# Kernel tuning notes

Hardware: AMD Instinct MI355X
Metric: run time of the kernel (lower is better)

## Reference

```python
import jax, jax.numpy as jnp
import numpy as np

HID = 1024
HEADS = 16
HEAD_DIM = HID // HEADS
MLP_HID = 4096
TEMB = 1024
EPS = 1e-6


def _ln(x):
    # LayerNorm without affine, eps=1e-6
    mu = jnp.mean(x, axis=-1, keepdims=True)
    var = jnp.var(x, axis=-1, keepdims=True)
    return (x - mu) * jax.lax.rsqrt(var + EPS)


def _modulate(x, shift, scale):
    return x * (1.0 + scale[:, None, :]) + shift[:, None, :]


def setup_inputs() -> dict:
    key = jax.random.key(0)
    ks = jax.random.split(key, 12)
    s = 0.02
    return {
        "x": jax.random.normal(ks[0], (8, 1024, HID), jnp.float32),
        "c": jax.random.normal(ks[1], (8, TEMB), jnp.float32),
        "W_qkv": jax.random.normal(ks[2], (HID, 3 * HID), jnp.float32) * s,
        "b_qkv": jnp.zeros((3 * HID,), jnp.float32),
        "W_proj": jax.random.normal(ks[3], (HID, HID), jnp.float32) * s,
        "b_proj": jnp.zeros((HID,), jnp.float32),
        "W_fc1": jax.random.normal(ks[4], (HID, MLP_HID), jnp.float32) * s,
        "b_fc1": jnp.zeros((MLP_HID,), jnp.float32),
        "W_fc2": jax.random.normal(ks[5], (MLP_HID, HID), jnp.float32) * s,
        "b_fc2": jnp.zeros((HID,), jnp.float32),
        "W_ada": jax.random.normal(ks[6], (TEMB, 6 * HID), jnp.float32) * s,
        "b_ada": jnp.zeros((6 * HID,), jnp.float32),
    }


def _attn(x, W_qkv, b_qkv, W_proj, b_proj):
    B, N, C = x.shape
    qkv = x @ W_qkv + b_qkv                      # [B,N,3C]
    qkv = qkv.reshape(B, N, 3, HEADS, HEAD_DIM)
    q, k, v = qkv[:, :, 0], qkv[:, :, 1], qkv[:, :, 2]  # [B,N,H,D]
    scale = HEAD_DIM ** -0.5
    logits = jnp.einsum('bnhd,bmhd->bhnm', q, k) * scale
    attn = jax.nn.softmax(logits, axis=-1)
    out = jnp.einsum('bhnm,bmhd->bnhd', attn, v).reshape(B, N, C)
    return out @ W_proj + b_proj


def reference(x, c, W_qkv, b_qkv, W_proj, b_proj, W_fc1, b_fc1, W_fc2, b_fc2, W_ada, b_ada):
    ada = jax.nn.silu(c) @ W_ada + b_ada          # [B,6C]
    shift_msa, scale_msa, gate_msa, shift_mlp, scale_mlp, gate_mlp = jnp.split(ada, 6, axis=1)

    h = _modulate(_ln(x), shift_msa, scale_msa)
    x = x + gate_msa[:, None, :] * _attn(h, W_qkv, b_qkv, W_proj, b_proj)

    h = _modulate(_ln(x), shift_mlp, scale_mlp)
    h = jax.nn.gelu(h @ W_fc1 + b_fc1, approximate=True) @ W_fc2 + b_fc2
    x = x + gate_mlp[:, None, :] * h
    return x
```

## Files before the change

kernel.cpp:

```cpp
#include <hip/hip_runtime.h>
#include <stdint.h>

typedef unsigned short u16;
typedef __attribute__((ext_vector_type(4))) float f32x4;
typedef __attribute__((ext_vector_type(8))) short bf16x8;
typedef bf16x8 bf16x8a __attribute__((may_alias));
typedef uint32_t u32a __attribute__((may_alias));

#define HID 1024
#define MLPD 4096
#define TEMB 1024
#define ADA_N 6144
#define SEQ 1024
#define BATCH 8
#define KCH 32
#define KCHLEN (TEMB / KCH)

__device__ __forceinline__ u16 f2bf_bits(float f) {
  uint32_t u = __float_as_uint(f);
  uint32_t r = (u + 0x7FFFu + ((u >> 16) & 1u)) >> 16;
  return (u16)r;
}

__device__ __forceinline__ float bf2f(u16 b) {
  return __uint_as_float(((uint32_t)b) << 16);
}

__device__ __forceinline__ uint32_t cvt_pk_bf16(float lo, float hi) {
  uint32_t r;
  asm("v_cvt_pk_bf16_f32 %0, %1, %2" : "=v"(r) : "v"(lo), "v"(hi));
  return r;
}

__device__ __forceinline__ float exp2_hw(float x) {
#if __has_builtin(__builtin_amdgcn_exp2f)
  return __builtin_amdgcn_exp2f(x);
#else
  return exp2f(x);
#endif
}

__device__ __forceinline__ void async_copy16(void* lds_dst, const void* g_src) {
  __builtin_amdgcn_global_load_lds(
      (const __attribute__((address_space(1))) void*)(uintptr_t)g_src,
      (__attribute__((address_space(3))) void*)(uint32_t)(uintptr_t)lds_dst,
      16, 0, 0);
}

__device__ __forceinline__ float gelu_tanh(float v) {
  float u = 0.7978845608028654f * (v + 0.044715f * v * v * v);
  float e = __expf(2.f * u);
  return v * e / (e + 1.f);
}

__global__ __launch_bounds__(256) void transpose_bf16(const float* __restrict__ W,
                                                      u16* __restrict__ Wt, int K, int N) {
  __shared__ float tile[32][33];
  int n0 = blockIdx.x * 32, k0 = blockIdx.y * 32;
  int tx = threadIdx.x & 31, ty = threadIdx.x >> 5;
#pragma unroll
  for (int i = 0; i < 4; i++)
    tile[ty + i * 8][tx] = W[(size_t)(k0 + ty + i * 8) * N + n0 + tx];
  __syncthreads();
#pragma unroll
  for (int i = 0; i < 4; i++)
    Wt[(size_t)(n0 + ty + i * 8) * K + k0 + tx] = f2bf_bits(tile[tx][ty + i * 8]);
}

__global__ __launch_bounds__(256) void ada_part(const float* __restrict__ c,
                                                const float* __restrict__ W,
                                                float* __restrict__ part) {
  __shared__ float sc[BATCH * KCHLEN];
  int t = threadIdx.x;
  int col = blockIdx.x * 256 + t;
  int kc = blockIdx.y;
  int k0 = kc * KCHLEN;
  for (int i = t; i < BATCH * KCHLEN; i += 256) {
    int b = i >> 5, kk = i & (KCHLEN - 1);
    float v = c[b * TEMB + k0 + kk];
    sc[i] = v / (1.f + __expf(-v));
  }
  __syncthreads();
  float acc[BATCH] = {};
  for (int kk = 0; kk < KCHLEN; kk++) {
    float w = W[(size_t)(k0 + kk) * ADA_N + col];
#pragma unroll
    for (int b = 0; b < BATCH; b++) acc[b] += sc[b * KCHLEN + kk] * w;
  }
#pragma unroll
  for (int b = 0; b < BATCH; b++)
    part[((size_t)kc * BATCH + b) * ADA_N + col] = acc[b];
}

__global__ __launch_bounds__(256) void ada_reduce(const float* __restrict__ part,
                                                  const float* __restrict__ bias,
                                                  float* __restrict__ out) {
  int i = blockIdx.x * 256 + threadIdx.x;
  int col = i % ADA_N, b = i / ADA_N;
  float s = bias[col];
#pragma unroll
  for (int kc = 0; kc < KCH; kc++)
    s += part[((size_t)kc * BATCH + b) * ADA_N + col];
  out[(size_t)b * ADA_N + col] = s;
}

__global__ __launch_bounds__(256) void ln_mod(const float* __restrict__ x,
                                              const float* __restrict__ ada,
                                              int shift_off, int scale_off,
                                              u16* __restrict__ h) {
  int row = blockIdx.x;
  int bb = row >> 10;
  int t = threadIdx.x;
  const float4 v = ((const float4*)(x + (size_t)row * HID))[t];
  float s = v.x + v.y + v.z + v.w;
  float sq = v.x * v.x + v.y * v.y + v.z * v.z + v.w * v.w;
#pragma unroll
  for (int off = 32; off >= 1; off >>= 1) {
    s += __shfl_xor(s, off);
    sq += __shfl_xor(sq, off);
  }
  __shared__ float red[8];
  int wid = t >> 6;
  if ((t & 63) == 0) { red[wid] = s; red[4 + wid] = sq; }
  __syncthreads();
  s = red[0] + red[1] + red[2] + red[3];
  sq = red[4] + red[5] + red[6] + red[7];
  float mu = s * (1.0f / HID);
  float rs = rsqrtf(sq * (1.0f / HID) - mu * mu + 1e-6f);
  const float4 sc = ((const float4*)(ada + (size_t)bb * ADA_N + scale_off))[t];
  const float4 sh = ((const float4*)(ada + (size_t)bb * ADA_N + shift_off))[t];
  ushort4 o;
  o.x = f2bf_bits((v.x - mu) * rs * (1.f + sc.x) + sh.x);
  o.y = f2bf_bits((v.y - mu) * rs * (1.f + sc.y) + sh.y);
  o.z = f2bf_bits((v.z - mu) * rs * (1.f + sc.z) + sh.z);
  o.w = f2bf_bits((v.w - mu) * rs * (1.f + sc.w) + sh.w);
  ((ushort4*)(h + (size_t)row * HID))[t] = o;
}


__device__ __forceinline__ void stage32(u16* dst, const u16* gsrc, int K, int koff, int t) {
#pragma unroll
  for (int i = 0; i < 2; ++i) {
    int slot = i * 256 + t;
    int row = slot >> 2, cp = slot & 3;
    const u16* src = gsrc + (size_t)row * K + koff + ((cp ^ ((row >> 1) & 3)) << 3);
    async_copy16(dst + slot * 8, src);
  }
}

#define LDSRD32(buf, row) \
  (*(const bf16x8a*)&(buf)[(row) * 32 + ((l4 ^ (((row) >> 1) & 3)) << 3)])

template <int EPI>
__global__ __launch_bounds__(256) void gemm2(const u16* __restrict__ A,
                                             const u16* __restrict__ Bt,
                                             const float* __restrict__ bias,
                                             void* __restrict__ Cout,
                                             const float* __restrict__ resid,
                                             const float* __restrict__ gate,
                                             int N, int K) {
  __shared__ u16 lds[24576];
  int t = threadIdx.x;
  int lane = t & 63, wid = t >> 6;
  int l15 = lane & 15, l4 = lane >> 4;
  int wr = wid >> 1, wc = wid & 1;
  int lid = blockIdx.x;
  int xcd = lid & 7, win = lid >> 3;
  int m0 = (xcd * 8 + (win & 7)) * 128;
  int n0 = (win >> 3) * 128;

  const u16* Abase = A + (size_t)m0 * K;
  const u16* Bbase = Bt + (size_t)n0 * K;
  f32x4 acc[4][4] = {};

  u16 *b0 = lds, *b1 = lds + 8192, *b2 = lds + 16384;
  int nt = K / 32;
  stage32(b0, Abase, K, 0, t);
  stage32(b0 + 4096, Bbase, K, 0, t);
  stage32(b1, Abase, K, 32, t);
  stage32(b1 + 4096, Bbase, K, 32, t);
  for (int ts = 0; ts < nt; ++ts) {
    if (ts + 2 < nt) {
      stage32(b2, Abase, K, (ts + 2) * 32, t);
      stage32(b2 + 4096, Bbase, K, (ts + 2) * 32, t);
      asm volatile("s_waitcnt vmcnt(8)" ::: "memory");
    } else if (ts + 1 < nt) {
      asm volatile("s_waitcnt vmcnt(4)" ::: "memory");
    } else {
      asm volatile("s_waitcnt vmcnt(0)" ::: "memory");
    }
    __builtin_amdgcn_s_barrier();
    bf16x8 af[4], bfr[4];
#pragma unroll
    for (int mi = 0; mi < 4; ++mi)
      af[mi] = LDSRD32(b0, wr * 64 + mi * 16 + l15);
#pragma unroll
    for (int ni = 0; ni < 4; ++ni)
      bfr[ni] = LDSRD32(b0 + 4096, wc * 64 + ni * 16 + l15);
#pragma unroll
    for (int mi = 0; mi < 4; ++mi)
#pragma unroll
      for (int ni = 0; ni < 4; ++ni)
        acc[mi][ni] = __builtin_amdgcn_mfma_f32_16x16x32_bf16(af[mi], bfr[ni], acc[mi][ni], 0, 0, 0);
    asm volatile("" ::: "memory");
    __builtin_amdgcn_s_barrier();
    u16* tp = b0; b0 = b1; b1 = b2; b2 = tp;
  }

  const int EST = 132;
  int bb = m0 >> 10;
#pragma unroll
  for (int ni = 0; ni < 4; ++ni) {
    int col = wc * 64 + ni * 16 + l15;
    float bv = bias[n0 + col];
    float gv = (EPI == 2) ? gate[(size_t)bb * ADA_N + n0 + col] : 0.f;
#pragma unroll
    for (int mi = 0; mi < 4; ++mi)
#pragma unroll
      for (int r = 0; r < 4; ++r) {
        int row = wr * 64 + mi * 16 + l4 * 4 + r;
        float v = acc[mi][ni][r] + bv;
        if (EPI == 1) v = gelu_tanh(v);
        if (EPI == 2) v = gv * v;
        lds[row * EST + col] = f2bf_bits(v);
      }
  }
  asm volatile("s_waitcnt lgkmcnt(0)" ::: "memory");
  __builtin_amdgcn_s_barrier();
  asm volatile("" ::: "memory");
  {
    int row = t >> 1, half = t & 1;
    size_t grow = (size_t)(m0 + row) * N + n0 + half * 64;
#pragma unroll
    for (int j = 0; j < 8; ++j) {
      bf16x8 v = *(const bf16x8a*)&lds[row * EST + half * 64 + j * 8];
      if (EPI == 2) {
        const float4* rp = (const float4*)&resid[grow + j * 8];
        float4 o0 = rp[0], o1 = rp[1];
        o0.x += bf2f((u16)v[0]); o0.y += bf2f((u16)v[1]);
        o0.z += bf2f((u16)v[2]); o0.w += bf2f((u16)v[3]);
        o1.x += bf2f((u16)v[4]); o1.y += bf2f((u16)v[5]);
        o1.z += bf2f((u16)v[6]); o1.w += bf2f((u16)v[7]);
        float4* op = (float4*)((float*)Cout + grow + j * 8);
        op[0] = o0; op[1] = o1;
      } else {
        *(bf16x8a*)((u16*)Cout + grow + j * 8) = v;
      }
    }
  }
}

__global__ __launch_bounds__(256, 3) void attn_kernel(const u16* __restrict__ qkv,
                                                      u16* __restrict__ O) {
  const int KSTR = 72, VSTR = 72, PSTR = 72;
  __shared__ u16 Ks[64 * 72];
  __shared__ u16 Vt[64 * 72];
  __shared__ u16 Plds[4 * 16 * 72];
  int t = threadIdx.x, lane = t & 63, wid = t >> 6;
  int l15 = lane & 15, l4 = lane >> 4;
  int work = ((blockIdx.x & 7) << 7) + (blockIdx.x >> 3);
  int bh = work >> 3, qt8 = work & 7;
  int b = bh >> 4, h = bh & 15;
  int bRow = b * SEQ;
  int hOff = h * 64;
  int q0 = qt8 * 128 + wid * 32;

  bf16x8 qr[2][2];
#pragma unroll
  for (int qt = 0; qt < 2; qt++) {
    const u16* qbase = qkv + (size_t)(bRow + q0 + qt * 16 + l15) * 3072 + hOff;
    qr[qt][0] = *(const bf16x8a*)(qbase + l4 * 8);
    qr[qt][1] = *(const bf16x8a*)(qbase + 32 + l4 * 8);
  }

  const float csc = 0.125f * 1.4426950408889634f;
  float mrow[2] = {-1e30f, -1e30f};
  float lsum[2] = {0.f, 0.f};
  f32x4 o[2][4] = {};
  u16* pw = Plds + wid * 16 * PSTR;

  for (int cc = 0; cc < 16; cc++) {
    int kv0 = cc * 64;
    __syncthreads();
#pragma unroll
    for (int i = 0; i < 2; i++) {
      int idx = i * 256 + t;
      int row = idx >> 3, ch = idx & 7;
      bf16x8 kk = *(const bf16x8a*)(qkv + (size_t)(bRow + kv0 + row) * 3072 + 1024 + hOff + ch * 8);
      *(bf16x8a*)&Ks[row * KSTR + ch * 8] = kk;
    }
#pragma unroll
    for (int i = 0; i < 2; i++) {
      int idx = i * 256 + t;
      int kv = idx >> 3, dc = idx & 7;
      bf16x8 vv = *(const bf16x8a*)(qkv + (size_t)(bRow + kv0 + kv) * 3072 + 2048 + hOff + dc * 8);
#pragma unroll
      for (int j = 0; j < 8; j++) {
        int jj = (j + dc) & 7;
        Vt[(dc * 8 + jj) * VSTR + kv] = ((const u16*)&vv)[jj];
      }
    }
    __syncthreads();

    bf16x8 ak[4][2];
#pragma unroll
    for (int kt = 0; kt < 4; kt++) {
      ak[kt][0] = *(const bf16x8a*)&Ks[(kt * 16 + l15) * KSTR + l4 * 8];
      ak[kt][1] = *(const bf16x8a*)&Ks[(kt * 16 + l15) * KSTR + 32 + l4 * 8];
    }
    f32x4 st[2][4];
#pragma unroll
    for (int qt = 0; qt < 2; qt++)
#pragma unroll
      for (int kt = 0; kt < 4; kt++) {
        f32x4 z = {0.f, 0.f, 0.f, 0.f};
        z = __builtin_amdgcn_mfma_f32_16x16x32_bf16(ak[kt][0], qr[qt][0], z, 0, 0, 0);
        z = __builtin_amdgcn_mfma_f32_16x16x32_bf16(ak[kt][1], qr[qt][1], z, 0, 0, 0);
        st[qt][kt] = z;
      }
    bf16x8 av[4][2];
#pragma unroll
    for (int dt = 0; dt < 4; dt++) {
      av[dt][0] = *(const bf16x8a*)&Vt[(dt * 16 + l15) * VSTR + l4 * 8];
      av[dt][1] = *(const bf16x8a*)&Vt[(dt * 16 + l15) * VSTR + 32 + l4 * 8];
    }

#pragma unroll
    for (int qt = 0; qt < 2; qt++) {
      float mx = st[qt][0][0];
#pragma unroll
      for (int kt = 0; kt < 4; kt++)
#pragma unroll
        for (int r = 0; r < 4; r++) mx = fmaxf(mx, st[qt][kt][r]);
      mx = fmaxf(mx, __shfl_xor(mx, 16));
      mx = fmaxf(mx, __shfl_xor(mx, 32));
      float mn = fmaxf(mrow[qt], mx * csc);
      float al = exp2_hw(mrow[qt] - mn);
      mrow[qt] = mn;
      float rs = 0.f;
#pragma unroll
      for (int kt = 0; kt < 4; kt++)
#pragma unroll
        for (int r = 0; r < 4; r++) {
          float p = exp2_hw(__builtin_fmaf(st[qt][kt][r], csc, -mn));
          st[qt][kt][r] = p;
          rs += p;
        }
      rs += __shfl_xor(rs, 16);
      rs += __shfl_xor(rs, 32);
      lsum[qt] = lsum[qt] * al + rs;
#pragma unroll
      for (int dt = 0; dt < 4; dt++) o[qt][dt] *= al;
#pragma unroll
      for (int kt = 0; kt < 4; kt++) {
#pragma unroll
        for (int hh = 0; hh < 2; hh++) {
          uint32_t pk = cvt_pk_bf16(st[qt][kt][2 * hh], st[qt][kt][2 * hh + 1]);
          *(u32a*)&pw[l15 * PSTR + kt * 16 + l4 * 4 + 2 * hh] = pk;
        }
      }
      asm volatile("s_waitcnt lgkmcnt(0)" ::: "memory");
      __builtin_amdgcn_sched_barrier(0);
      bf16x8 bp0 = *(const bf16x8a*)&pw[l15 * PSTR + l4 * 8];
      bf16x8 bp1 = *(const bf16x8a*)&pw[l15 * PSTR + 32 + l4 * 8];
#pragma unroll
      for (int dt = 0; dt < 4; dt++) {
        o[qt][dt] = __builtin_amdgcn_mfma_f32_16x16x32_bf16(av[dt][0], bp0, o[qt][dt], 0, 0, 0);
        o[qt][dt] = __builtin_amdgcn_mfma_f32_16x16x32_bf16(av[dt][1], bp1, o[qt][dt], 0, 0, 0);
      }
      asm volatile("s_waitcnt lgkmcnt(0)" ::: "memory");
      __builtin_amdgcn_sched_barrier(0);
    }
  }
#pragma unroll
  for (int qt = 0; qt < 2; qt++) {
    float inv = 1.f / lsum[qt];
    u16* orow = O + (size_t)(bRow + q0 + qt * 16 + l15) * HID + hOff;
#pragma unroll
    for (int dt = 0; dt < 4; dt++) {
      uint2 w;
      w.x = cvt_pk_bf16(o[qt][dt][0] * inv, o[qt][dt][1] * inv);
      w.y = cvt_pk_bf16(o[qt][dt][2] * inv, o[qt][dt][3] * inv);
      *(uint2*)(orow + dt * 16 + l4 * 4) = w;
    }
  }
}

extern "C" void kernel_launch(void* const* d_in, const int* in_sizes, int n_in,
                              void* d_out, int out_size, void* d_ws, size_t ws_size,
                              hipStream_t stream) {
  const float* x      = (const float*)d_in[0];
  const float* c      = (const float*)d_in[1];
  const float* W_qkv  = (const float*)d_in[2];
  const float* b_qkv  = (const float*)d_in[3];
  const float* W_proj = (const float*)d_in[4];
  const float* b_proj = (const float*)d_in[5];
  const float* W_fc1  = (const float*)d_in[6];
  const float* b_fc1  = (const float*)d_in[7];
  const float* W_fc2  = (const float*)d_in[8];
  const float* b_fc2  = (const float*)d_in[9];
  const float* W_ada  = (const float*)d_in[10];
  const float* b_ada  = (const float*)d_in[11];
  float* out = (float*)d_out;
  char* ws = (char*)d_ws;

  float* ada  = (float*)(ws + 0);
  u16* WtQKV  = (u16*)(ws + 196608);
  u16* WtP    = (u16*)(ws + 6488064);
  u16* WtF1   = (u16*)(ws + 8585216);
  u16* WtF2   = (u16*)(ws + 16973824);
  u16* hbuf   = (u16*)(ws + 25362432);
  u16* big    = (u16*)(ws + 42139648);
  float* apart = (float*)(ws + 42139648);

  transpose_bf16<<<dim3(3072 / 32, 1024 / 32), 256, 0, stream>>>(W_qkv, WtQKV, 1024, 3072);
  transpose_bf16<<<dim3(1024 / 32, 1024 / 32), 256, 0, stream>>>(W_proj, WtP, 1024, 1024);
  transpose_bf16<<<dim3(4096 / 32, 1024 / 32), 256, 0, stream>>>(W_fc1, WtF1, 1024, 4096);
  transpose_bf16<<<dim3(1024 / 32, 4096 / 32), 256, 0, stream>>>(W_fc2, WtF2, 4096, 1024);
  ada_part<<<dim3(ADA_N / 256, KCH), 256, 0, stream>>>(c, W_ada, apart);
  ada_reduce<<<(BATCH * ADA_N) / 256, 256, 0, stream>>>(apart, b_ada, ada);
  ln_mod<<<8192, 256, 0, stream>>>(x, ada, 0, 1024, hbuf);
  gemm2<0><<<1536, 256, 0, stream>>>(hbuf, WtQKV, b_qkv, big, nullptr, nullptr, 3072, 1024);
  attn_kernel<<<1024, 256, 0, stream>>>(big, hbuf);
  gemm2<2><<<512, 256, 0, stream>>>(hbuf, WtP, b_proj, out, x, ada + 2048, 1024, 1024);
  ln_mod<<<8192, 256, 0, stream>>>(out, ada, 3072, 4096, hbuf);
  gemm2<1><<<2048, 256, 0, stream>>>(hbuf, WtF1, b_fc1, big, nullptr, nullptr, 4096, 1024);
  gemm2<2><<<512, 256, 0, stream>>>(big, WtF2, b_fc2, out, out, ada + 5120, 1024, 4096);
}
```

Measured before the change: 426.1 us.

## Replace 128x128 GEMM with 256x256-tile, 512-thread pipelined GEMM

Replaces the 128x128x32 triple-buffered GEMM with a 256x256 output tile, a K-step of 64 and 8 waves per block. A and B loads for the next steps are interleaved between four MFMA quarter-phases, and s_setprio is raised around the MFMA bursts. The larger tile raises arithmetic intensity and cuts global traffic per FLOP. In exchange it uses 128KB of LDS and many accumulator registers per wave, and it gives far fewer blocks: only 128 for the 1024-wide N GEMMs, which may underfill the 256 CUs. The epilogue is split into two 128-row passes to reuse LDS.

```diff
diff --git a/kernel.cpp b/kernel.cpp
--- a/kernel.cpp
+++ b/kernel.cpp
@@ -138,115 +138,145 @@
 }
 
 
-__device__ __forceinline__ void stage32(u16* dst, const u16* gsrc, int K, int koff, int t) {
+__device__ __forceinline__ void stage_chunk(u16* dstTile, int h, const u16* gsrc,
+                                            int K, int koff, int t) {
 #pragma unroll
   for (int i = 0; i < 2; ++i) {
-    int slot = i * 256 + t;
-    int row = slot >> 2, cp = slot & 3;
-    const u16* src = gsrc + (size_t)row * K + koff + ((cp ^ ((row >> 1) & 3)) << 3);
-    async_copy16(dst + slot * 8, src);
-  }
-}
-
-#define LDSRD32(buf, row) \
-  (*(const bf16x8a*)&(buf)[(row) * 32 + ((l4 ^ (((row) >> 1) & 3)) << 3)])
+    int slot = i * 512 + t;
+    int row = (h << 7) + (slot >> 3);
+    int cp = slot & 7;
+    const u16* src = gsrc + (size_t)row * K + koff + ((cp ^ (row & 7)) << 3);
+    async_copy16(dstTile + (h << 13) + slot * 8, src);
+  }
+}
+
+#define LDSRD64(buf, row, kk) \
+  (*(const bf16x8a*)&(buf)[(row) * 64 + ((((kk) * 4 + l4) ^ ((row) & 7)) << 3)])
+
+#define G256_QUAD(p)                                                          \
+  {                                                                           \
+    bf16x8 af0[2][2];                                                         \
+    _Pragma("unroll")                                                         \
+    for (int i = 0; i < 2; ++i)                                               \
+      _Pragma("unroll")                                                       \
+      for (int kk = 0; kk < 2; ++kk)                                          \
+        af0[i][kk] = LDSRD64(Ac, wr * 128 + ((p) * 2 + i) * 16 + l15, kk);    \
+    __builtin_amdgcn_s_setprio(1);                                            \
+    _Pragma("unroll")                                                         \
+    for (int i = 0; i < 2; ++i)                                               \
+      _Pragma("unroll")                                                       \
+      for (int ni = 0; ni < 4; ++ni) {                                        \
+        acc[(p) * 2 + i][ni] = __builtin_amdgcn_mfma_f32_16x16x32_bf16(       \
+            af0[i][0], bf[ni][0], acc[(p) * 2 + i][ni], 0, 0, 0);             \
+        acc[(p) * 2 + i][ni] = __builtin_amdgcn_mfma_f32_16x16x32_bf16(       \
+            af0[i][1], bf[ni][1], acc[(p) * 2 + i][ni], 0, 0, 0);             \
+      }                                                                       \
+    __builtin_amdgcn_s_setprio(0);                                            \
+    asm volatile("" ::: "memory");                                            \
+    __builtin_amdgcn_s_barrier();                                             \
+  }
 
 template <int EPI>
-__global__ __launch_bounds__(256) void gemm2(const u16* __restrict__ A,
-                                             const u16* __restrict__ Bt,
-                                             const float* __restrict__ bias,
-                                             void* __restrict__ Cout,
-                                             const float* __restrict__ resid,
-                                             const float* __restrict__ gate,
-                                             int N, int K) {
-  __shared__ u16 lds[24576];
+__global__ __launch_bounds__(512, 2) void gemm256(const u16* __restrict__ A,
+                                                  const u16* __restrict__ Bt,
+                                                  const float* __restrict__ bias,
+                                                  void* __restrict__ Cout,
+                                                  const float* __restrict__ resid,
+                                                  const float* __restrict__ gate,
+                                                  int N, int K) {
+  __shared__ u16 lds[65536];
   int t = threadIdx.x;
   int lane = t & 63, wid = t >> 6;
   int l15 = lane & 15, l4 = lane >> 4;
-  int wr = wid >> 1, wc = wid & 1;
+  int wr = wid >> 2, wc = wid & 3;
   int lid = blockIdx.x;
   int xcd = lid & 7, win = lid >> 3;
-  int m0 = (xcd * 8 + (win & 7)) * 128;
-  int n0 = (win >> 3) * 128;
+  int m0 = (xcd * 4 + (win & 3)) * 256;
+  int n0 = (win >> 2) * 256;
 
   const u16* Abase = A + (size_t)m0 * K;
   const u16* Bbase = Bt + (size_t)n0 * K;
-  f32x4 acc[4][4] = {};
-
-  u16 *b0 = lds, *b1 = lds + 8192, *b2 = lds + 16384;
-  int nt = K / 32;
-  stage32(b0, Abase, K, 0, t);
-  stage32(b0 + 4096, Bbase, K, 0, t);
-  stage32(b1, Abase, K, 32, t);
-  stage32(b1 + 4096, Bbase, K, 32, t);
-  for (int ts = 0; ts < nt; ++ts) {
-    if (ts + 2 < nt) {
-      stage32(b2, Abase, K, (ts + 2) * 32, t);
-      stage32(b2 + 4096, Bbase, K, (ts + 2) * 32, t);
-      asm volatile("s_waitcnt vmcnt(8)" ::: "memory");
-    } else if (ts + 1 < nt) {
-      asm volatile("s_waitcnt vmcnt(4)" ::: "memory");
-    } else {
-      asm volatile("s_waitcnt vmcnt(0)" ::: "memory");
-    }
+  f32x4 acc[8][4] = {};
+  int nt = K / 64;
+
+  stage_chunk(lds + 32768, 0, Bbase, K, 0, t);
+  stage_chunk(lds + 32768, 1, Bbase, K, 0, t);
+  stage_chunk(lds, 0, Abase, K, 0, t);
+  stage_chunk(lds, 1, Abase, K, 0, t);
+  stage_chunk(lds + 49152, 0, Bbase, K, 64, t);
+  stage_chunk(lds + 49152, 1, Bbase, K, 64, t);
+
+  for (int T = 0; T < nt; ++T) {
+    int db = T & 1;
+    u16* Ac = db ? lds + 16384 : lds;
+    u16* Bc = db ? lds + 49152 : lds + 32768;
+    u16* An = db ? lds : lds + 16384;
+    if (T + 1 < nt) stage_chunk(An, 0, Abase, K, (T + 1) * 64, t);
+    if (T == nt - 1) asm volatile("s_waitcnt vmcnt(0)" ::: "memory");
+    else             asm volatile("s_waitcnt vmcnt(6)" ::: "memory");
     __builtin_amdgcn_s_barrier();
-    bf16x8 af[4], bfr[4];
-#pragma unroll
-    for (int mi = 0; mi < 4; ++mi)
-      af[mi] = LDSRD32(b0, wr * 64 + mi * 16 + l15);
+    bf16x8 bf[4][2];
 #pragma unroll
     for (int ni = 0; ni < 4; ++ni)
-      bfr[ni] = LDSRD32(b0 + 4096, wc * 64 + ni * 16 + l15);
-#pragma unroll
-    for (int mi = 0; mi < 4; ++mi)
-#pragma unroll
-      for (int ni = 0; ni < 4; ++ni)
-        acc[mi][ni] = __builtin_amdgcn_mfma_f32_16x16x32_bf16(af[mi], bfr[ni], acc[mi][ni], 0, 0, 0);
+#pragma unroll
+      for (int kk = 0; kk < 2; ++kk)
+        bf[ni][kk] = LDSRD64(Bc, wc * 64 + ni * 16 + l15, kk);
+    G256_QUAD(0)
+    if (T + 1 < nt) stage_chunk(An, 1, Abase, K, (T + 1) * 64, t);
+    G256_QUAD(1)
+    if (T + 2 < nt) stage_chunk(Bc, 0, Bbase, K, (T + 2) * 64, t);
+    G256_QUAD(2)
+    if (T + 2 < nt) stage_chunk(Bc, 1, Bbase, K, (T + 2) * 64, t);
+    G256_QUAD(3)
+  }
+
+  const int EST = 260;
+  int bb = m0 >> 10;
+#pragma unroll
+  for (int rp = 0; rp < 2; ++rp) {
+    if (wr == rp) {
+#pragma unroll
+      for (int ni = 0; ni < 4; ++ni) {
+        int col = wc * 64 + ni * 16 + l15;
+        float bv = bias[n0 + col];
+        float gv = (EPI == 2) ? gate[(size_t)bb * ADA_N + n0 + col] : 0.f;
+#pragma unroll
+        for (int mi = 0; mi < 8; ++mi)
+#pragma unroll
+          for (int r = 0; r < 4; ++r) {
+            int row = mi * 16 + l4 * 4 + r;
+            float v = acc[mi][ni][r] + bv;
+            if (EPI == 1) v = gelu_tanh(v);
+            if (EPI == 2) v = gv * v;
+            lds[row * EST + col] = f2bf_bits(v);
+          }
+      }
+    }
+    asm volatile("s_waitcnt lgkmcnt(0)" ::: "memory");
+    __builtin_amdgcn_s_barrier();
+    asm volatile("" ::: "memory");
+    {
+      int row = t >> 2, q = t & 3;
+      size_t grow = (size_t)(m0 + rp * 128 + row) * N + n0 + q * 64;
+#pragma unroll
+      for (int j = 0; j < 8; ++j) {
+        bf16x8 v = *(const bf16x8a*)&lds[row * EST + q * 64 + j * 8];
+        if (EPI == 2) {
+          const float4* rpn = (const float4*)&resid[grow + j * 8];
+          float4 o0 = rpn[0], o1 = rpn[1];
+          o0.x += bf2f((u16)v[0]); o0.y += bf2f((u16)v[1]);
+          o0.z += bf2f((u16)v[2]); o0.w += bf2f((u16)v[3]);
+          o1.x += bf2f((u16)v[4]); o1.y += bf2f((u16)v[5]);
+          o1.z += bf2f((u16)v[6]); o1.w += bf2f((u16)v[7]);
+          float4* op = (float4*)((float*)Cout + grow + j * 8);
+          op[0] = o0; op[1] = o1;
+        } else {
+          *(bf16x8a*)((u16*)Cout + grow + j * 8) = v;
+        }
+      }
+    }
     asm volatile("" ::: "memory");
     __builtin_amdgcn_s_barrier();
-    u16* tp = b0; b0 = b1; b1 = b2; b2 = tp;
-  }
-
-  const int EST = 132;
-  int bb = m0 >> 10;
-#pragma unroll
-  for (int ni = 0; ni < 4; ++ni) {
-    int col = wc * 64 + ni * 16 + l15;
-    float bv = bias[n0 + col];
-    float gv = (EPI == 2) ? gate[(size_t)bb * ADA_N + n0 + col] : 0.f;
-#pragma unroll
-    for (int mi = 0; mi < 4; ++mi)
-#pragma unroll
-      for (int r = 0; r < 4; ++r) {
-        int row = wr * 64 + mi * 16 + l4 * 4 + r;
-        float v = acc[mi][ni][r] + bv;
-        if (EPI == 1) v = gelu_tanh(v);
-        if (EPI == 2) v = gv * v;
-        lds[row * EST + col] = f2bf_bits(v);
-      }
-  }
-  asm volatile("s_waitcnt lgkmcnt(0)" ::: "memory");
-  __builtin_amdgcn_s_barrier();
-  asm volatile("" ::: "memory");
-  {
-    int row = t >> 1, half = t & 1;
-    size_t grow = (size_t)(m0 + row) * N + n0 + half * 64;
-#pragma unroll
-    for (int j = 0; j < 8; ++j) {
-      bf16x8 v = *(const bf16x8a*)&lds[row * EST + half * 64 + j * 8];
-      if (EPI == 2) {
-        const float4* rp = (const float4*)&resid[grow + j * 8];
-        float4 o0 = rp[0], o1 = rp[1];
-        o0.x += bf2f((u16)v[0]); o0.y += bf2f((u16)v[1]);
-        o0.z += bf2f((u16)v[2]); o0.w += bf2f((u16)v[3]);
-        o1.x += bf2f((u16)v[4]); o1.y += bf2f((u16)v[5]);
-        o1.z += bf2f((u16)v[6]); o1.w += bf2f((u16)v[7]);
-        float4* op = (float4*)((float*)Cout + grow + j * 8);
-        op[0] = o0; op[1] = o1;
-      } else {
-        *(bf16x8a*)((u16*)Cout + grow + j * 8) = v;
-      }
-    }
   }
 }
 
@@ -420,10 +450,10 @@
   ada_part<<<dim3(ADA_N / 256, KCH), 256, 0, stream>>>(c, W_ada, apart);
   ada_reduce<<<(BATCH * ADA_N) / 256, 256, 0, stream>>>(apart, b_ada, ada);
   ln_mod<<<8192, 256, 0, stream>>>(x, ada, 0, 1024, hbuf);
-  gemm2<0><<<1536, 256, 0, stream>>>(hbuf, WtQKV, b_qkv, big, nullptr, nullptr, 3072, 1024);
+  gemm256<0><<<384, 512, 0, stream>>>(hbuf, WtQKV, b_qkv, big, nullptr, nullptr, 3072, 1024);
   attn_kernel<<<1024, 256, 0, stream>>>(big, hbuf);
-  gemm2<2><<<512, 256, 0, stream>>>(hbuf, WtP, b_proj, out, x, ada + 2048, 1024, 1024);
+  gemm256<2><<<128, 512, 0, stream>>>(hbuf, WtP, b_proj, out, x, ada + 2048, 1024, 1024);
   ln_mod<<<8192, 256, 0, stream>>>(out, ada, 3072, 4096, hbuf);
-  gemm2<1><<<2048, 256, 0, stream>>>(hbuf, WtF1, b_fc1, big, nullptr, nullptr, 4096, 1024);
-  gemm2<2><<<512, 256, 0, stream>>>(big, WtF2, b_fc2, out, out, ada + 5120, 1024, 4096);
-}
+  gemm256<1><<<512, 512, 0, stream>>>(hbuf, WtF1, b_fc1, big, nullptr, nullptr, 4096, 1024);
+  gemm256<2><<<128, 512, 0, stream>>>(big, WtF2, b_fc2, out, out, ada + 5120, 1024, 4096);
+}
```

Measured after the change: 504.6 us. 18.4% more time.
